# Kernel tuning notes

Hardware: AMD Instinct MI355X
Metric: run time of the kernel (lower is better)

## Reference

```python
import jax, jax.numpy as jnp
import numpy as np

IN_DIM = 64      # hidden_size / num_attention_heads
OUT_DIM = 256    # number of random features
SIGMA = IN_DIM ** 0.25


def setup_inputs() -> dict:
    key = jax.random.key(0)
    k1, k2, k3, k4 = jax.random.split(key, 4)
    B, S, D = 64, 4096, IN_DIM  # bsz*n_heads, seq_len, head_size
    q = jax.random.normal(k1, (B, S, D), dtype=jnp.float32)
    k = jax.random.normal(k2, (B, S, D), dtype=jnp.float32)
    v = jax.random.normal(k3, (B, S, D), dtype=jnp.float32)
    # orthogonal-ish random feature matrix [OUT_DIM, IN_DIM] (orthonormal columns per block)
    w = jax.random.normal(k4, (OUT_DIM, IN_DIM), dtype=jnp.float32)
    qmat, _ = jnp.linalg.qr(w.T)  # [IN_DIM, IN_DIM] per... use full QR of transpose then tile
    blocks = []
    for i in range(OUT_DIM // IN_DIM):
        g = jax.random.normal(jax.random.fold_in(k4, i), (IN_DIM, IN_DIM), dtype=jnp.float32)
        qb, _ = jnp.linalg.qr(g)
        blocks.append(qb)
    weight = jnp.concatenate(blocks, axis=0)  # [OUT_DIM, IN_DIM], row blocks orthogonal
    return {"q": q, "k": k, "v": v, "weight": weight}


def _orf_map_exp(x, weight, is_query):
    # x: [B, S, D], weight: [F, D]
    x_norm_sqr = jnp.sum(x * x, axis=-1, keepdims=True) * 0.5      # [B,S,1]
    x_proj = jnp.einsum('bsd,fd->bsf', x, weight)                  # [B,S,F]
    normalizer = jnp.max(x_proj, axis=-1, keepdims=True)           # [B,S,1]
    if not is_query:
        normalizer = jnp.max(normalizer, axis=-2, keepdims=True)   # [B,1,1]
    return jnp.exp(x_proj - x_norm_sqr - normalizer) * (weight.shape[0] ** -0.5)


def reference(q, k, v, weight):
    q = q / SIGMA
    k = k / SIGMA
    k = k - jnp.mean(k, axis=-2, keepdims=True)
    phi_q = _orf_map_exp(q, weight, True)    # [B,S,F]
    phi_k = _orf_map_exp(k, weight, False)   # [B,S,F]
    # linear attention: O(S * F * D)
    k_sum = jnp.sum(phi_k, axis=-2)                               # [B,F]
    kv = jnp.einsum('bsf,bsd->bfd', phi_k, v)                     # [B,F,D]
    deno = jnp.maximum(jnp.einsum('bsf,bf->bs', phi_q, k_sum), 1e-4)  # [B,S]
    out = jnp.einsum('bsf,bfd->bsd', phi_q, kv) / deno[..., None]     # [B,S,D]
    return out
```

## Files before the change

### kernel.cpp

```cpp
#include <hip/hip_runtime.h>

#define BB 64
#define SS 4096
#define DD 64
#define FF 256
#define INVS 0.35355339059327373f
#define FSCALE 0.0625f

#define KV_OFF_F    0
#define KSUM_OFF_F  (BB*FF*DD)
#define MKEY_OFF_F  (KSUM_OFF_F + BB*FF)
#define NKEY_OFF_F  (MKEY_OFF_F + BB)
#define MSUM_OFF_F  (NKEY_OFF_F + BB)
#define WS_ZERO_F   (MSUM_OFF_F + BB*DD)
#define WS_ZERO_BYTES (WS_ZERO_F * 4)

typedef _Float16 f16;
typedef __attribute__((ext_vector_type(4))) _Float16 f16x4;
typedef __attribute__((ext_vector_type(8))) _Float16 f16x8;
typedef __attribute__((ext_vector_type(4))) float f32x4;

__device__ __forceinline__ unsigned fkey(float f) {
    unsigned b = __float_as_uint(f);
    return (f < 0.0f) ? ~b : (b | 0x80000000u);
}
__device__ __forceinline__ float funkey(unsigned k) {
    return (k & 0x80000000u) ? __uint_as_float(k ^ 0x80000000u) : __uint_as_float(~k);
}
__device__ __forceinline__ void splitf(float x, f16& h, f16& l) {
    h = (f16)x;
    l = (f16)(x - (float)h);
}

__global__ __launch_bounds__(256) void k_stats(const float* __restrict__ kin,
                                               float* __restrict__ msum,
                                               unsigned* __restrict__ nkey) {
    const int b = blockIdx.y, chunk = blockIdx.x;
    const int t = threadIdx.x, row = t >> 4, c16 = t & 15;
    const float4* kg = (const float4*)(kin + (size_t)b * (SS * DD));
    float4 cacc = make_float4(0.f, 0.f, 0.f, 0.f);
    float nmax = 0.f;
    const int s0 = chunk * 256;
    #pragma unroll 4
    for (int it = 0; it < 16; ++it) {
        const int s = s0 + it * 16 + row;
        float4 x = kg[s * 16 + c16];
        cacc.x += x.x; cacc.y += x.y; cacc.z += x.z; cacc.w += x.w;
        float sq = x.x * x.x + x.y * x.y + x.z * x.z + x.w * x.w;
        #pragma unroll
        for (int off = 1; off <= 8; off <<= 1) sq += __shfl_xor(sq, off);
        nmax = fmaxf(nmax, sq);
    }
    __shared__ float csum[64];
    __shared__ float wm[4];
    if (t < 64) csum[t] = 0.f;
    __syncthreads();
    atomicAdd(&csum[c16 * 4 + 0], cacc.x);
    atomicAdd(&csum[c16 * 4 + 1], cacc.y);
    atomicAdd(&csum[c16 * 4 + 2], cacc.z);
    atomicAdd(&csum[c16 * 4 + 3], cacc.w);
    nmax = fmaxf(nmax, __shfl_xor(nmax, 16));
    nmax = fmaxf(nmax, __shfl_xor(nmax, 32));
    if ((t & 63) == 0) wm[t >> 6] = nmax;
    __syncthreads();
    if (t < 64) atomicAdd(&msum[b * DD + t], csum[t]);
    if (t == 0) {
        float mx = fmaxf(fmaxf(wm[0], wm[1]), fmaxf(wm[2], wm[3]));
        atomicMax(&nkey[b], fkey(mx));
    }
}

__global__ __launch_bounds__(512, 1) void k_kv(const float* __restrict__ kin,
                                               const float* __restrict__ vin,
                                               const float* __restrict__ w,
                                               float* __restrict__ ws) {
    float* kv = ws + KV_OFF_F;
    float* ksum = ws + KSUM_OFF_F;
    unsigned* mkey = (unsigned*)ws + MKEY_OFF_F;
    const unsigned* nkey = (const unsigned*)ws + NKEY_OFF_F;
    const float* msum = ws + MSUM_OFF_F;

    const int b = blockIdx.y, chunk = blockIdx.x;
    const int t = threadIdx.x;
    const int wid = t >> 6, l = t & 63, quad = l >> 4, m = l & 15;
    const int st = wid & 1, fgroup = wid >> 1;

    __shared__ __align__(16) f16 kH[32 * 72], kL[32 * 72];
    __shared__ __align__(16) f16 vTH[64 * 40], vTL[64 * 40];
    __shared__ __align__(16) f16 pTH[256 * 40], pTL[256 * 40];
    __shared__ __align__(16) float cS[32];
    __shared__ __align__(16) float muL[64];
    __shared__ float ksumL[256];
    __shared__ float redw[8];
    __shared__ float mhatL;

    if (t < 64) {
        float mv = msum[b * DD + t] * (1.0f / 4096.0f);
        muL[t] = mv;
        float sq = mv * mv;
        #pragma unroll
        for (int off = 32; off; off >>= 1) sq += __shfl_xor(sq, off);
        if (t == 0) mhatL = (sqrtf(funkey(nkey[b])) + sqrtf(sq)) * INVS;
    }
    if (t < 256) ksumL[t] = 0.f;

    f16x8 wbH[4][2], wbL[4][2];
    #pragma unroll
    for (int ff = 0; ff < 4; ++ff) {
        #pragma unroll
        for (int ks = 0; ks < 2; ++ks) {
            const float* wp = w + (((fgroup * 4 + ff) * 16 + m) * 64 + ks * 32 + quad * 8);
            float4 x0 = *(const float4*)wp;
            float4 x1 = *(const float4*)(wp + 4);
            f16 h, lo;
            splitf(x0.x, h, lo); wbH[ff][ks][0] = h; wbL[ff][ks][0] = lo;
            splitf(x0.y, h, lo); wbH[ff][ks][1] = h; wbL[ff][ks][1] = lo;
            splitf(x0.z, h, lo); wbH[ff][ks][2] = h; wbL[ff][ks][2] = lo;
            splitf(x0.w, h, lo); wbH[ff][ks][3] = h; wbL[ff][ks][3] = lo;
            splitf(x1.x, h, lo); wbH[ff][ks][4] = h; wbL[ff][ks][4] = lo;
            splitf(x1.y, h, lo); wbH[ff][ks][5] = h; wbL[ff][ks][5] = lo;
            splitf(x1.z, h, lo); wbH[ff][ks][6] = h; wbL[ff][ks][6] = lo;
            splitf(x1.w, h, lo); wbH[ff][ks][7] = h; wbL[ff][ks][7] = lo;
        }
    }
    __syncthreads();
    const float mhat = mhatL;
    const int srow = t >> 4, scol = t & 15;
    const float4 mu4 = *(const float4*)&muL[scol * 4];

    f32x4 acc2[8];
    #pragma unroll
    for (int i = 0; i < 8; ++i) acc2[i] = (f32x4){0.f, 0.f, 0.f, 0.f};
    float dmax = -1e30f;

    const int rbase = chunk * 1024;
    const float4* kg = (const float4*)(kin + (size_t)b * (SS * DD));
    const float4* vg = (const float4*)(vin + (size_t)b * (SS * DD));

    float4 k4 = kg[(rbase + srow) * 16 + scol];
    float4 v4 = vg[(rbase + srow) * 16 + scol];

    for (int it = 0; it < 32; ++it) {
        float4 kc;
        kc.x = (k4.x - mu4.x) * INVS; kc.y = (k4.y - mu4.y) * INVS;
        kc.z = (k4.z - mu4.z) * INVS; kc.w = (k4.w - mu4.w) * INVS;
        float sq = kc.x * kc.x + kc.y * kc.y + kc.z * kc.z + kc.w * kc.w;
        #pragma unroll
        for (int off = 1; off <= 8; off <<= 1) sq += __shfl_xor(sq, off);
        if (scol == 0) cS[srow] = 0.5f * sq;
        {
            f16x4 khv, klv;
            f16 h, lo;
            splitf(kc.x, h, lo); khv[0] = h; klv[0] = lo;
            splitf(kc.y, h, lo); khv[1] = h; klv[1] = lo;
            splitf(kc.z, h, lo); khv[2] = h; klv[2] = lo;
            splitf(kc.w, h, lo); khv[3] = h; klv[3] = lo;
            *(f16x4*)&kH[srow * 72 + scol * 4] = khv;
            *(f16x4*)&kL[srow * 72 + scol * 4] = klv;
        }
        #pragma unroll
        for (int u = 0; u < 4; ++u) {
            float vv = (&v4.x)[u];
            f16 vh, vl;
            splitf(vv, vh, vl);
            vTH[(scol * 4 + u) * 40 + srow] = vh;
            vTL[(scol * 4 + u) * 40 + srow] = vl;
        }
        __syncthreads();

        f16x8 aH[2], aL[2];
        #pragma unroll
        for (int ks = 0; ks < 2; ++ks) {
            aH[ks] = *(const f16x8*)&kH[(st * 16 + m) * 72 + ks * 32 + quad * 8];
            aL[ks] = *(const f16x8*)&kL[(st * 16 + m) * 72 + ks * 32 + quad * 8];
        }
        const float4 c4 = *(const float4*)&cS[st * 16 + quad * 4];
        const int s0 = st * 16 + quad * 4;
        #pragma unroll
        for (int ff = 0; ff < 4; ++ff) {
            f32x4 acc = (f32x4){0.f, 0.f, 0.f, 0.f};
            #pragma unroll
            for (int ks = 0; ks < 2; ++ks) {
                acc = __builtin_amdgcn_mfma_f32_16x16x32_f16(aH[ks], wbH[ff][ks], acc, 0, 0, 0);
                acc = __builtin_amdgcn_mfma_f32_16x16x32_f16(aH[ks], wbL[ff][ks], acc, 0, 0, 0);
                acc = __builtin_amdgcn_mfma_f32_16x16x32_f16(aL[ks], wbH[ff][ks], acc, 0, 0, 0);
            }
            float ksp = 0.f;
            f16x4 phv, plv;
            #pragma unroll
            for (int r = 0; r < 4; ++r) {
                float d = acc[r];
                dmax = fmaxf(dmax, d);
                float p = __expf(d - (&c4.x)[r] - mhat) * FSCALE;
                ksp += p;
                f16 h, lo;
                splitf(p, h, lo);
                phv[r] = h; plv[r] = lo;
            }
            const int f = (fgroup * 4 + ff) * 16 + m;
            *(f16x4*)&pTH[f * 40 + s0] = phv;
            *(f16x4*)&pTL[f * 40 + s0] = plv;
            ksp += __shfl_xor(ksp, 16);
            ksp += __shfl_xor(ksp, 32);
            if (l < 16) atomicAdd(&ksumL[(fgroup * 4 + ff) * 16 + l], ksp);
        }
        __syncthreads();

        if (it < 31) {
            k4 = kg[(rbase + (it + 1) * 32 + srow) * 16 + scol];
            v4 = vg[(rbase + (it + 1) * 32 + srow) * 16 + scol];
        }

        f16x8 aH2[2], aL2[2], bH2[4], bL2[4];
        #pragma unroll
        for (int tt = 0; tt < 2; ++tt) {
            const int f = (wid * 2 + tt) * 16 + m;
            aH2[tt] = *(const f16x8*)&pTH[f * 40 + quad * 8];
            aL2[tt] = *(const f16x8*)&pTL[f * 40 + quad * 8];
        }
        #pragma unroll
        for (int dtile = 0; dtile < 4; ++dtile) {
            const int d = dtile * 16 + m;
            bH2[dtile] = *(const f16x8*)&vTH[d * 40 + quad * 8];
            bL2[dtile] = *(const f16x8*)&vTL[d * 40 + quad * 8];
        }
        #pragma unroll
        for (int tt = 0; tt < 2; ++tt) {
            #pragma unroll
            for (int dtile = 0; dtile < 4; ++dtile) {
                f32x4 a = acc2[tt * 4 + dtile];
                a = __builtin_amdgcn_mfma_f32_16x16x32_f16(aH2[tt], bH2[dtile], a, 0, 0, 0);
                a = __builtin_amdgcn_mfma_f32_16x16x32_f16(aH2[tt], bL2[dtile], a, 0, 0, 0);
                a = __builtin_amdgcn_mfma_f32_16x16x32_f16(aL2[tt], bH2[dtile], a, 0, 0, 0);
                acc2[tt * 4 + dtile] = a;
            }
        }
        __syncthreads();
    }

    #pragma unroll
    for (int tt = 0; tt < 2; ++tt) {
        #pragma unroll
        for (int dtile = 0; dtile < 4; ++dtile) {
            #pragma unroll
            for (int r = 0; r < 4; ++r) {
                const int f = (wid * 2 + tt) * 16 + quad * 4 + r;
                const int d = dtile * 16 + m;
                atomicAdd(&kv[((size_t)b * FF + f) * DD + d], acc2[tt * 4 + dtile][r]);
            }
        }
    }
    if (t < 256) atomicAdd(&ksum[b * FF + t], ksumL[t]);
    #pragma unroll
    for (int off = 32; off; off >>= 1) dmax = fmaxf(dmax, __shfl_xor(dmax, off));
    if (l == 0) redw[wid] = dmax;
    __syncthreads();
    if (t == 0) {
        float mx = redw[0];
        #pragma unroll
        for (int i = 1; i < 8; ++i) mx = fmaxf(mx, redw[i]);
        atomicMax(&mkey[b], fkey(mx));
    }
}

__global__ __launch_bounds__(512, 2) void k_out(const float* __restrict__ qin,
                                                const float* __restrict__ w,
                                                const float* __restrict__ ws,
                                                float* __restrict__ outp) {
    const float* kv = ws + KV_OFF_F;
    const float* ksum = ws + KSUM_OFF_F;
    const unsigned* mkey = (const unsigned*)ws + MKEY_OFF_F;
    const unsigned* nkey = (const unsigned*)ws + NKEY_OFF_F;
    const float* msum = ws + MSUM_OFF_F;

    const int b = blockIdx.y, chunk = blockIdx.x, t = threadIdx.x;
    const int wid = t >> 6, l = t & 63, quad = l >> 4, m = l & 15;
    const int st = wid & 1, fgroup = wid >> 1;
    const int dt = wid >> 1;

    __shared__ __align__(16) f16 qH[32 * 72], qL[32 * 72];
    __shared__ __align__(16) f16 pH[32 * 264], pL[32 * 264];
    __shared__ __align__(16) float oL[32 * 68];
    __shared__ float cS[32], mqL[32];
    __shared__ float ksL[256];
    __shared__ float denoP[4][32], dmaxP[4][32];
    __shared__ float scaleL[32];
    __shared__ float abL;

    if (t < 64) {
        float mv = msum[b * DD + t] * (1.0f / 4096.0f);
        float sq = mv * mv;
        #pragma unroll
        for (int off = 32; off; off >>= 1) sq += __shfl_xor(sq, off);
        if (t == 0) {
            float mhat = (sqrtf(funkey(nkey[b])) + sqrtf(sq)) * INVS;
            abL = __expf(mhat - funkey(mkey[b]));
        }
    }
    if (t < 256) ksL[t] = ksum[b * FF + t];

    f16x8 wbH[4][2], wbL[4][2];
    #pragma unroll
    for (int ff = 0; ff < 4; ++ff) {
        #pragma unroll
        for (int ks = 0; ks < 2; ++ks) {
            const float* wp = w + (((fgroup * 4 + ff) * 16 + m) * 64 + ks * 32 + quad * 8);
            float4 x0 = *(const float4*)wp;
            float4 x1 = *(const float4*)(wp + 4);
            f16 h, lo;
            splitf(x0.x, h, lo); wbH[ff][ks][0] = h; wbL[ff][ks][0] = lo;
            splitf(x0.y, h, lo); wbH[ff][ks][1] = h; wbL[ff][ks][1] = lo;
            splitf(x0.z, h, lo); wbH[ff][ks][2] = h; wbL[ff][ks][2] = lo;
            splitf(x0.w, h, lo); wbH[ff][ks][3] = h; wbL[ff][ks][3] = lo;
            splitf(x1.x, h, lo); wbH[ff][ks][4] = h; wbL[ff][ks][4] = lo;
            splitf(x1.y, h, lo); wbH[ff][ks][5] = h; wbL[ff][ks][5] = lo;
            splitf(x1.z, h, lo); wbH[ff][ks][6] = h; wbL[ff][ks][6] = lo;
            splitf(x1.w, h, lo); wbH[ff][ks][7] = h; wbL[ff][ks][7] = lo;
        }
    }

    f16x8 kvH[8], kvL[8];
    {
        const float* kvg = kv + (size_t)b * (FF * DD) + dt * 16 + m;
        #pragma unroll
        for (int ks = 0; ks < 8; ++ks) {
            #pragma unroll
            for (int j = 0; j < 8; ++j) {
                float x = kvg[(ks * 32 + quad * 8 + j) * 64];
                f16 h, lo;
                splitf(x, h, lo);
                kvH[ks][j] = h; kvL[ks][j] = lo;
            }
        }
    }
    __syncthreads();

    const int srow = t >> 4, scol = t & 15;
    const int rbase = chunk * 512;
    const float4* qg = (const float4*)qin + (size_t)b * (SS * 16);
    float4* og = (float4*)outp + (size_t)b * (SS * 16);

    float4 q4 = qg[(rbase + srow) * 16 + scol];

    for (int it = 0; it < 16; ++it) {
        float4 qs;
        qs.x = q4.x * INVS; qs.y = q4.y * INVS;
        qs.z = q4.z * INVS; qs.w = q4.w * INVS;
        float sq = qs.x * qs.x + qs.y * qs.y + qs.z * qs.z + qs.w * qs.w;
        #pragma unroll
        for (int off = 1; off <= 8; off <<= 1) sq += __shfl_xor(sq, off);
        if (scol == 0) { cS[srow] = 0.5f * sq; mqL[srow] = sqrtf(sq); }
        {
            f16x4 hv, lv;
            f16 h, lo;
            splitf(qs.x, h, lo); hv[0] = h; lv[0] = lo;
            splitf(qs.y, h, lo); hv[1] = h; lv[1] = lo;
            splitf(qs.z, h, lo); hv[2] = h; lv[2] = lo;
            splitf(qs.w, h, lo); hv[3] = h; lv[3] = lo;
            *(f16x4*)&qH[srow * 72 + scol * 4] = hv;
            *(f16x4*)&qL[srow * 72 + scol * 4] = lv;
        }
        __syncthreads();

        f16x8 bqH[2], bqL[2];
        #pragma unroll
        for (int ks = 0; ks < 2; ++ks) {
            bqH[ks] = *(const f16x8*)&qH[(st * 16 + m) * 72 + ks * 32 + quad * 8];
            bqL[ks] = *(const f16x8*)&qL[(st * 16 + m) * 72 + ks * 32 + quad * 8];
        }
        const float cs = cS[st * 16 + m];
        const float mq = mqL[st * 16 + m];
        float dpart = 0.f, dmax = -1e30f;
        #pragma unroll
        for (int ff = 0; ff < 4; ++ff) {
            f32x4 acc = (f32x4){0.f, 0.f, 0.f, 0.f};
            #pragma unroll
            for (int ks = 0; ks < 2; ++ks) {
                acc = __builtin_amdgcn_mfma_f32_16x16x32_f16(wbH[ff][ks], bqH[ks], acc, 0, 0, 0);
                acc = __builtin_amdgcn_mfma_f32_16x16x32_f16(wbH[ff][ks], bqL[ks], acc, 0, 0, 0);
                acc = __builtin_amdgcn_mfma_f32_16x16x32_f16(wbL[ff][ks], bqH[ks], acc, 0, 0, 0);
            }
            const int f0 = (fgroup * 4 + ff) * 16 + quad * 4;
            const float4 ksv = *(const float4*)&ksL[f0];
            f16x4 phv, plv;
            #pragma unroll
            for (int r = 0; r < 4; ++r) {
                float d = acc[r];
                dmax = fmaxf(dmax, d);
                float p = __expf(d - cs - mq);
                dpart = fmaf(p, (&ksv.x)[r], dpart);
                f16 h, lo;
                splitf(p, h, lo);
                phv[r] = h; plv[r] = lo;
            }
            *(f16x4*)&pH[(st * 16 + m) * 264 + f0] = phv;
            *(f16x4*)&pL[(st * 16 + m) * 264 + f0] = plv;
        }
        dpart += __shfl_xor(dpart, 16);
        dpart += __shfl_xor(dpart, 32);
        dmax = fmaxf(dmax, __shfl_xor(dmax, 16));
        dmax = fmaxf(dmax, __shfl_xor(dmax, 32));
        if (l < 16) {
            denoP[fgroup][st * 16 + l] = dpart;
            dmaxP[fgroup][st * 16 + l] = dmax;
        }
        __syncthreads();

        if (t < 32) {
            float dn0 = denoP[0][t] + denoP[1][t] + denoP[2][t] + denoP[3][t];
            float mt = fmaxf(fmaxf(dmaxP[0][t], dmaxP[1][t]),
                             fmaxf(dmaxP[2][t], dmaxP[3][t]));
            float A = abL * __expf(mqL[t] - mt) * FSCALE;
            float dn = fmaxf(A * dn0, 1e-4f);
            scaleL[t] = A / dn;
        }
        if (it < 15) q4 = qg[(rbase + (it + 1) * 32 + srow) * 16 + scol];

        f32x4 acc2 = (f32x4){0.f, 0.f, 0.f, 0.f};
        #pragma unroll
        for (int ks = 0; ks < 8; ++ks) {
            f16x8 paH = *(const f16x8*)&pH[(st * 16 + m) * 264 + ks * 32 + quad * 8];
            f16x8 paL = *(const f16x8*)&pL[(st * 16 + m) * 264 + ks * 32 + quad * 8];
            acc2 = __builtin_amdgcn_mfma_f32_16x16x32_f16(paH, kvH[ks], acc2, 0, 0, 0);
            acc2 = __builtin_amdgcn_mfma_f32_16x16x32_f16(paH, kvL[ks], acc2, 0, 0, 0);
            acc2 = __builtin_amdgcn_mfma_f32_16x16x32_f16(paL, kvH[ks], acc2, 0, 0, 0);
        }
        #pragma unroll
        for (int r = 0; r < 4; ++r)
            oL[(st * 16 + quad * 4 + r) * 68 + dt * 16 + m] = acc2[r];
        __syncthreads();

        {
            float4 ov = *(const float4*)&oL[srow * 68 + scol * 4];
            float s = scaleL[srow];
            og[(rbase + it * 32 + srow) * 16 + scol] =
                make_float4(ov.x * s, ov.y * s, ov.z * s, ov.w * s);
        }
    }
}

extern "C" void kernel_launch(void* const* d_in, const int* in_sizes, int n_in,
                              void* d_out, int out_size, void* d_ws, size_t ws_size,
                              hipStream_t stream) {
    (void)in_sizes; (void)n_in; (void)out_size; (void)ws_size;
    const float* q = (const float*)d_in[0];
    const float* k = (const float*)d_in[1];
    const float* v = (const float*)d_in[2];
    const float* w = (const float*)d_in[3];
    float* out = (float*)d_out;
    float* ws = (float*)d_ws;

    hipMemsetAsync(d_ws, 0, WS_ZERO_BYTES, stream);
    k_stats<<<dim3(16, 64), 256, 0, stream>>>(k, ws + MSUM_OFF_F, (unsigned*)ws + NKEY_OFF_F);
    k_kv<<<dim3(4, 64), 512, 0, stream>>>(k, v, w, ws);
    k_out<<<dim3(8, 64), 512, 0, stream>>>(q, w, ws, out);
}
```

Before: 379.4 us.

## Double k_kv grid, swizzle LDS tiles, and keep ksum partials in registers

Splits each batch's sequence into 8 chunks of 512 rows instead of 4 of 1024, so k_kv launches 512 blocks instead of 256, and raises launch bounds to allow more resident blocks per CU. It XOR-swizzles the vT and pT shared-memory layouts to reduce LDS bank conflicts on the transposed stores and loads. It replaces the per-iteration shared-memory atomicAdd for ksum with per-thread register accumulation that is flushed once to global memory. The trade-offs are twice as many global atomics for kv, and register pressure from the higher launch-bounds minimum, which could cause spills.

```diff
diff --git a/kernel.cpp b/kernel.cpp
--- a/kernel.cpp
+++ b/kernel.cpp
@@ -70,7 +70,7 @@
     }
 }
 
-__global__ __launch_bounds__(512, 1) void k_kv(const float* __restrict__ kin,
+__global__ __launch_bounds__(512, 4) void k_kv(const float* __restrict__ kin,
                                                const float* __restrict__ vin,
                                                const float* __restrict__ w,
                                                float* __restrict__ ws) {
@@ -90,7 +90,6 @@
     __shared__ __align__(16) f16 pTH[256 * 40], pTL[256 * 40];
     __shared__ __align__(16) float cS[32];
     __shared__ __align__(16) float muL[64];
-    __shared__ float ksumL[256];
     __shared__ float redw[8];
     __shared__ float mhatL;
 
@@ -102,7 +101,6 @@
         for (int off = 32; off; off >>= 1) sq += __shfl_xor(sq, off);
         if (t == 0) mhatL = (sqrtf(funkey(nkey[b])) + sqrtf(sq)) * INVS;
     }
-    if (t < 256) ksumL[t] = 0.f;
 
     f16x8 wbH[4][2], wbL[4][2];
     #pragma unroll
@@ -131,16 +129,20 @@
     f32x4 acc2[8];
     #pragma unroll
     for (int i = 0; i < 8; ++i) acc2[i] = (f32x4){0.f, 0.f, 0.f, 0.f};
+    float ksacc[4] = {0.f, 0.f, 0.f, 0.f};
     float dmax = -1e30f;
 
-    const int rbase = chunk * 1024;
+    const int rbase = chunk * 512;
     const float4* kg = (const float4*)(kin + (size_t)b * (SS * DD));
     const float4* vg = (const float4*)(vin + (size_t)b * (SS * DD));
 
     float4 k4 = kg[(rbase + srow) * 16 + scol];
     float4 v4 = vg[(rbase + srow) * 16 + scol];
 
-    for (int it = 0; it < 32; ++it) {
+    const int vgW = scol & 3;
+    const int sG = srow >> 3, sIn = srow & 7;
+
+    for (int it = 0; it < 16; ++it) {
         float4 kc;
         kc.x = (k4.x - mu4.x) * INVS; kc.y = (k4.y - mu4.y) * INVS;
         kc.z = (k4.z - mu4.z) * INVS; kc.w = (k4.w - mu4.w) * INVS;
@@ -163,8 +165,9 @@
             float vv = (&v4.x)[u];
             f16 vh, vl;
             splitf(vv, vh, vl);
-            vTH[(scol * 4 + u) * 40 + srow] = vh;
-            vTL[(scol * 4 + u) * 40 + srow] = vl;
+            const int idx = (scol * 4 + u) * 40 + ((sG ^ vgW) << 3) + sIn;
+            vTH[idx] = vh;
+            vTL[idx] = vl;
         }
         __syncthreads();
 
@@ -175,7 +178,9 @@
             aL[ks] = *(const f16x8*)&kL[(st * 16 + m) * 72 + ks * 32 + quad * 8];
         }
         const float4 c4 = *(const float4*)&cS[st * 16 + quad * 4];
-        const int s0 = st * 16 + quad * 4;
+        const int mG = (m >> 2) & 3;
+        const int pG = ((st * 2 + (quad >> 1)) ^ mG);
+        const int pOff = (pG << 3) + ((quad & 1) << 2);
         #pragma unroll
         for (int ff = 0; ff < 4; ++ff) {
             f32x4 acc = (f32x4){0.f, 0.f, 0.f, 0.f};
@@ -198,15 +203,15 @@
                 phv[r] = h; plv[r] = lo;
             }
             const int f = (fgroup * 4 + ff) * 16 + m;
-            *(f16x4*)&pTH[f * 40 + s0] = phv;
-            *(f16x4*)&pTL[f * 40 + s0] = plv;
+            *(f16x4*)&pTH[f * 40 + pOff] = phv;
+            *(f16x4*)&pTL[f * 40 + pOff] = plv;
             ksp += __shfl_xor(ksp, 16);
             ksp += __shfl_xor(ksp, 32);
-            if (l < 16) atomicAdd(&ksumL[(fgroup * 4 + ff) * 16 + l], ksp);
-        }
-        __syncthreads();
-
-        if (it < 31) {
+            ksacc[ff] += ksp;
+        }
+        __syncthreads();
+
+        if (it < 15) {
             k4 = kg[(rbase + (it + 1) * 32 + srow) * 16 + scol];
             v4 = vg[(rbase + (it + 1) * 32 + srow) * 16 + scol];
         }
@@ -215,14 +220,16 @@
         #pragma unroll
         for (int tt = 0; tt < 2; ++tt) {
             const int f = (wid * 2 + tt) * 16 + m;
-            aH2[tt] = *(const f16x8*)&pTH[f * 40 + quad * 8];
-            aL2[tt] = *(const f16x8*)&pTL[f * 40 + quad * 8];
+            const int off = f * 40 + ((quad ^ mG) << 3);
+            aH2[tt] = *(const f16x8*)&pTH[off];
+            aL2[tt] = *(const f16x8*)&pTL[off];
         }
         #pragma unroll
         for (int dtile = 0; dtile < 4; ++dtile) {
             const int d = dtile * 16 + m;
-            bH2[dtile] = *(const f16x8*)&vTH[d * 40 + quad * 8];
-            bL2[dtile] = *(const f16x8*)&vTL[d * 40 + quad * 8];
+            const int off = d * 40 + ((quad ^ mG) << 3);
+            bH2[dtile] = *(const f16x8*)&vTH[off];
+            bL2[dtile] = *(const f16x8*)&vTL[off];
         }
         #pragma unroll
         for (int tt = 0; tt < 2; ++tt) {
@@ -250,7 +257,11 @@
             }
         }
     }
-    if (t < 256) atomicAdd(&ksum[b * FF + t], ksumL[t]);
+    if (l < 16) {
+        #pragma unroll
+        for (int ff = 0; ff < 4; ++ff)
+            atomicAdd(&ksum[b * FF + (fgroup * 4 + ff) * 16 + l], ksacc[ff]);
+    }
     #pragma unroll
     for (int off = 32; off; off >>= 1) dmax = fmaxf(dmax, __shfl_xor(dmax, off));
     if (l == 0) redw[wid] = dmax;
@@ -452,6 +463,6 @@
 
     hipMemsetAsync(d_ws, 0, WS_ZERO_BYTES, stream);
     k_stats<<<dim3(16, 64), 256, 0, stream>>>(k, ws + MSUM_OFF_F, (unsigned*)ws + NKEY_OFF_F);
-    k_kv<<<dim3(4, 64), 512, 0, stream>>>(k, v, w, ws);
+    k_kv<<<dim3(8, 64), 512, 0, stream>>>(k, v, w, ws);
     k_out<<<dim3(8, 64), 512, 0, stream>>>(q, w, ws, out);
 }
```

After: 488.0 us. 28.6% more time.
